# Performance work log

Hardware: AMD Instinct MI355X
Metric: run time of the kernel (lower is better)

## Reference

```python
import jax, jax.numpy as jnp
import numpy as np

D = 1024
H = 4
HD = D // H
B = 256
L = 64
DILATIONS = (1, 4, 8, 16)


def setup_inputs() -> dict:
    key = jax.random.key(0)
    ks = jax.random.split(key, 12)
    s = 1.0 / np.sqrt(D)
    return {
        "x": jax.random.normal(ks[0], (B, D), jnp.float32),
        "hist": jax.random.normal(ks[1], (L, B, D), jnp.float32),
        "Wq": jax.random.normal(ks[2], (D, D), jnp.float32) * s,
        "bq": jnp.zeros((D,), jnp.float32),
        "Wk": jax.random.normal(ks[3], (D, D), jnp.float32) * s,
        "bk": jnp.zeros((D,), jnp.float32),
        "Wv": jax.random.normal(ks[4], (D, D), jnp.float32) * s,
        "bv": jnp.zeros((D,), jnp.float32),
        "Wo": jax.random.normal(ks[5], (D, D), jnp.float32) * s,
        "bo": jnp.zeros((D,), jnp.float32),
        "dil_w": jnp.full((len(DILATIONS),), 1.0 / len(DILATIONS), jnp.float32),
        "gamma": jnp.ones((D,), jnp.float32),
        "beta": jnp.zeros((D,), jnp.float32),
    }


def reference(x, hist, Wq, bq, Wk, bk, Wv, bv, Wo, bo, dil_w, gamma, beta):
    scale = 1.0 / np.sqrt(HD)
    q = (x @ Wq + bq).reshape(B, H, HD)  # (B, H, HD)
    attended = []
    for d in DILATIONS:
        # history frames at stride d, concatenated along dim 0 (faithful to torch.cat)
        frames = hist[::d].reshape(-1, D)              # (T', D), T' = ceil(L/d)*B
        k = (frames @ Wk + bk).reshape(-1, H, HD)      # (T', H, HD)
        v = (frames @ Wv + bv).reshape(-1, H, HD)
        s = jnp.einsum('bhd,thd->bht', q, k) * scale   # (B, H, T')
        a = jax.nn.softmax(s, axis=-1)
        attended.append(jnp.einsum('bht,thd->bhd', a, v).reshape(B, D))
    w = jax.nn.softmax(dil_w, axis=0)
    combined = sum(w[i] * attended[i] for i in range(len(DILATIONS)))
    y = x + combined @ Wo + bo
    mu = jnp.mean(y, axis=-1, keepdims=True)
    var = jnp.var(y, axis=-1, keepdims=True)
    return (y - mu) / jnp.sqrt(var + 1e-5) * gamma + beta
```

## Files before the change

### kernel.cpp

```cpp
#include <hip/hip_runtime.h>


#define DD    1024
#define TALL  16384

typedef _Float16 half8  __attribute__((ext_vector_type(8)));
typedef _Float16 half4v __attribute__((ext_vector_type(4)));
typedef float    floatx4 __attribute__((ext_vector_type(4)));
typedef unsigned int u32;

static const size_t OFF_WOT  = 0;
static const size_t OFF_WV16 = 2097152;
static const size_t OFF_WK16 = 4194304;
static const size_t OFF_WQ16 = 6291456;
static const size_t OFF_XB   = 8388608;
static const size_t OFF_G    = 8912896;
static const size_t OFF_WVOT = 11010048;
static const size_t OFF_WQKT = 19398656;
static const size_t OFF_BVWO = 27787264;
static const size_t OFF_BQK  = 27791360;
static const size_t OFF_PHR  = 27807744;
static const size_t OFF_OPP  = 29904896;
static const size_t OFF_HB   = 38293504;
static const size_t OFF_HT   = 71848960;
static const size_t OFF_S    = 105403392;

__device__ __forceinline__ size_t chunk16_off(int g) {
  if (g < 4)  return (size_t)g * 2097152;
  if (g < 8)  return 19398656 + (size_t)(g - 4) * 2097152;
  if (g < 12) return 29904896 + (size_t)(g - 8) * 2097152;
  return 38293504 + (size_t)(g - 12) * 2097152;
}

__device__ __forceinline__ void gl_lds16(const void* g, void* l) {
  __builtin_amdgcn_global_load_lds((const __attribute__((address_space(1))) u32*)g,
                                   (__attribute__((address_space(3))) u32*)l, 16, 0, 0);
}

__global__ void prep_kernel(const float* __restrict__ Wo, const float* __restrict__ Wv,
                            const float* __restrict__ Wk, const float* __restrict__ Wq,
                            const float* __restrict__ x, const float* __restrict__ hist,
                            _Float16* __restrict__ WoT, _Float16* __restrict__ Wv16,
                            _Float16* __restrict__ Wk16, _Float16* __restrict__ Wq16,
                            _Float16* __restrict__ xb, _Float16* __restrict__ histb,
                            _Float16* __restrict__ histT) {
  int bid = blockIdx.x, tid = threadIdx.x;
  if (bid < 1024) {
    int k0 = (bid & 31) * 32, n0 = (bid >> 5) * 32;
    __shared__ float t32[32][33];
    int tx = tid & 31, ty = tid >> 5;
#pragma unroll
    for (int i = 0; i < 4; i++) {
      int r = ty + i * 8;
      t32[r][tx] = Wo[(size_t)(k0 + r) * DD + n0 + tx];
    }
    __syncthreads();
#pragma unroll
    for (int i = 0; i < 4; i++) {
      int r = ty + i * 8;
      WoT[(size_t)(n0 + r) * DD + k0 + tx] = (_Float16)t32[tx][r];
    }
  } else if (bid < 4352) {
    const float* src; _Float16* dst; size_t i;
    if (bid < 2048)      { src = Wv; dst = Wv16; i = (size_t)(bid - 1024) * 256 + tid; }
    else if (bid < 3072) { src = Wk; dst = Wk16; i = (size_t)(bid - 2048) * 256 + tid; }
    else if (bid < 4096) { src = Wq; dst = Wq16; i = (size_t)(bid - 3072) * 256 + tid; }
    else                 { src = x;  dst = xb;   i = (size_t)(bid - 4096) * 256 + tid; }
    float4 v = ((const float4*)src)[i];
    half4v h = {(_Float16)v.x, (_Float16)v.y, (_Float16)v.z, (_Float16)v.w};
    *(half4v*)(dst + 4 * i) = h;
  } else {
    int tb = bid - 4352;
    int t0 = (tb & 255) * 64, f0 = (tb >> 8) * 64;
    __shared__ _Float16 lt[64][72];
    int r = tid >> 2, c0 = (tid & 3) * 16;
    half8 s0, s1;
#pragma unroll
    for (int i = 0; i < 4; i++) {
      float4 v = *(const float4*)&hist[(size_t)(t0 + r) * 1024 + f0 + c0 + i * 4];
      half4v h = {(_Float16)v.x, (_Float16)v.y, (_Float16)v.z, (_Float16)v.w};
      *(half4v*)&lt[r][c0 + i * 4] = h;
      if (i < 2) { s0[i*4]=h[0]; s0[i*4+1]=h[1]; s0[i*4+2]=h[2]; s0[i*4+3]=h[3]; }
      else { s1[(i-2)*4]=h[0]; s1[(i-2)*4+1]=h[1]; s1[(i-2)*4+2]=h[2]; s1[(i-2)*4+3]=h[3]; }
    }
    *(half8*)&histb[(size_t)(t0 + r) * 1024 + f0 + c0] = s0;
    *(half8*)&histb[(size_t)(t0 + r) * 1024 + f0 + c0 + 8] = s1;
    __syncthreads();
    int fr = tid >> 2, tc0 = (tid & 3) * 16;
    half8 o0, o1;
#pragma unroll
    for (int j = 0; j < 8; j++) { o0[j] = lt[tc0 + j][fr]; o1[j] = lt[tc0 + 8 + j][fr]; }
    *(half8*)&histT[(size_t)(f0 + fr) * TALL + t0 + tc0] = o0;
    *(half8*)&histT[(size_t)(f0 + fr) * TALL + t0 + tc0 + 8] = o1;
  }
}

__device__ __forceinline__ void gemm_core(const _Float16* __restrict__ A, size_t lda,
                                          const _Float16* __restrict__ B, size_t ldb,
                                          int kIters, _Float16* As, _Float16* Bs,
                                          int tid, floatx4 acc[4][4]) {
  int lane = tid & 63, w = tid >> 6;
  int l15 = lane & 15, quad = lane >> 4;
  int wm = (w >> 1) * 64, wn = (w & 1) * 64;
  int swz = ((tid & 3) ^ ((tid >> 3) & 3)) * 8;
  int pch = (quad ^ ((l15 >> 1) & 3)) * 8;
  const char* gA0 = (const char*)(A + (size_t)(tid >> 2) * lda + swz);
  const char* gA1 = (const char*)(A + ((size_t)(tid >> 2) + 64) * lda + swz);
  const char* gB0 = (const char*)(B + (size_t)(tid >> 2) * ldb + swz);
  const char* gB1 = (const char*)(B + ((size_t)(tid >> 2) + 64) * ldb + swz);
  _Float16* lA = As + w * 512;
  _Float16* lB = Bs + w * 512;
#define GC_STAGE(buf, k)                                    \
  do {                                                      \
    size_t off_ = (size_t)(k) * 64;                         \
    gl_lds16(gA0 + off_, lA + (buf) * 4096);                \
    gl_lds16(gA1 + off_, lA + (buf) * 4096 + 2048);         \
    gl_lds16(gB0 + off_, lB + (buf) * 4096);                \
    gl_lds16(gB1 + off_, lB + (buf) * 4096 + 2048);         \
  } while (0)
#define GC_STEP(buf, k)                                                       \
  do {                                                                        \
    if ((k) + 1 < kIters) asm volatile("s_waitcnt vmcnt(4)" ::: "memory");    \
    else                  asm volatile("s_waitcnt vmcnt(0)" ::: "memory");    \
    asm volatile("s_barrier" ::: "memory");                                   \
    const _Float16* Ac_ = As + (buf) * 4096;                                  \
    const _Float16* Bc_ = Bs + (buf) * 4096;                                  \
    half8 a_[4];                                                              \
    _Pragma("unroll")                                                         \
    for (int mi = 0; mi < 4; mi++)                                            \
      a_[mi] = *(const half8*)&Ac_[(wm + mi * 16 + l15) * 32 + pch];          \
    _Pragma("unroll")                                                         \
    for (int ni = 0; ni < 4; ni++) {                                          \
      half8 b8_ = *(const half8*)&Bc_[(wn + ni * 16 + l15) * 32 + pch];       \
      _Pragma("unroll")                                                       \
      for (int mi = 0; mi < 4; mi++)                                          \
        acc[mi][ni] = __builtin_amdgcn_mfma_f32_16x16x32_f16(a_[mi], b8_,     \
                                                             acc[mi][ni], 0, 0, 0); \
    }                                                                         \
    asm volatile("s_waitcnt lgkmcnt(0)" ::: "memory");                        \
    asm volatile("s_barrier" ::: "memory");                                   \
    if ((k) + 2 < kIters) GC_STAGE(buf, (k) + 2);                             \
  } while (0)
  GC_STAGE(0, 0);
  GC_STAGE(1, 1);
  for (int kk = 0; kk < kIters; kk += 2) {
    GC_STEP(0, kk);
    GC_STEP(1, kk + 1);
  }
#undef GC_STEP
#undef GC_STAGE
}

__device__ __forceinline__ void gemm256_core(const _Float16* __restrict__ A, size_t lda,
                                             const _Float16* __restrict__ B, size_t ldb,
                                             int nT, _Float16* As, _Float16* Bs,
                                             int tid, floatx4 acc[8][4]) {
  int lane = tid & 63, w = tid >> 6;
  int l15 = lane & 15, quad = lane >> 4;
  int wr = w >> 2, wc = w & 3;
  int pch = (quad ^ ((l15 >> 1) & 3)) * 8;
  int srow = tid >> 2;
  int schunk = (tid & 3) ^ ((tid >> 3) & 3);
  const char* gA0 = (const char*)(A + (size_t)srow * lda + schunk * 8);
  const char* gA1 = (const char*)(A + (size_t)(srow + 128) * lda + schunk * 8);
  const char* gB0 = (const char*)(B + (size_t)srow * ldb + schunk * 8);
  const char* gB1 = (const char*)(B + (size_t)(srow + 128) * ldb + schunk * 8);
  _Float16* lA = As + w * 512;
  _Float16* lB = Bs + w * 512;
#define STA256(buf, t)                                        \
  do { size_t o_ = (size_t)(t) * 64;                          \
    gl_lds16(gA0 + o_, lA + (buf) * 8192);                    \
    gl_lds16(gA1 + o_, lA + (buf) * 8192 + 4096);             \
  } while (0)
#define STB256(buf, t)                                        \
  do { size_t o_ = (size_t)(t) * 64;                          \
    gl_lds16(gB0 + o_, lB + (buf) * 8192);                    \
    gl_lds16(gB1 + o_, lB + (buf) * 8192 + 4096);             \
  } while (0)
  STA256(0, 0); STB256(0, 0);
  if (nT > 1) { STA256(1, 1); STB256(1, 1); }
  if (nT > 2) { STA256(2, 2); STB256(2, 2); }
  for (int t = 0; t < nT; ++t) {
    int buf = t & 3;
    if (t + 2 < nT)      asm volatile("s_waitcnt vmcnt(8)" ::: "memory");
    else if (t + 1 < nT) asm volatile("s_waitcnt vmcnt(4)" ::: "memory");
    else                 asm volatile("s_waitcnt vmcnt(0)" ::: "memory");
    asm volatile("s_barrier" ::: "memory");
    const _Float16* Ac = As + buf * 8192;
    const _Float16* Bc = Bs + buf * 8192;
    half8 b8[4], a8[4];
#pragma unroll
    for (int ni = 0; ni < 4; ni++)
      b8[ni] = *(const half8*)&Bc[(wc * 64 + ni * 16 + l15) * 32 + pch];
#pragma unroll
    for (int mi = 0; mi < 4; mi++)
      a8[mi] = *(const half8*)&Ac[(wr * 128 + mi * 16 + l15) * 32 + pch];
    if (t + 3 < nT) STA256((t + 3) & 3, t + 3);
    asm volatile("s_barrier" ::: "memory");
    asm volatile("s_waitcnt lgkmcnt(0)" ::: "memory");
    __builtin_amdgcn_s_setprio(1);
#pragma unroll
    for (int mi = 0; mi < 4; mi++)
#pragma unroll
      for (int ni = 0; ni < 4; ni++)
        acc[mi][ni] = __builtin_amdgcn_mfma_f32_16x16x32_f16(a8[mi], b8[ni], acc[mi][ni], 0, 0, 0);
    __builtin_amdgcn_s_setprio(0);
    asm volatile("s_barrier" ::: "memory");
#pragma unroll
    for (int mi = 0; mi < 4; mi++)
      a8[mi] = *(const half8*)&Ac[(wr * 128 + 64 + mi * 16 + l15) * 32 + pch];
    if (t + 3 < nT) STB256((t + 3) & 3, t + 3);
    asm volatile("s_barrier" ::: "memory");
    asm volatile("s_waitcnt lgkmcnt(0)" ::: "memory");
    __builtin_amdgcn_s_setprio(1);
#pragma unroll
    for (int mi = 0; mi < 4; mi++)
#pragma unroll
      for (int ni = 0; ni < 4; ni++)
        acc[4 + mi][ni] = __builtin_amdgcn_mfma_f32_16x16x32_f16(a8[mi], b8[ni], acc[4 + mi][ni], 0, 0, 0);
    __builtin_amdgcn_s_setprio(0);
    asm volatile("s_barrier" ::: "memory");
  }
#undef STA256
#undef STB256
}

template <bool OUTF32>
__launch_bounds__(256, 3)
__global__ void gemm_f16_kernel(const _Float16* __restrict__ A, size_t lda, size_t aoffz,
                                const _Float16* __restrict__ B, size_t ldb, size_t boffz,
                                int kIters, const float* __restrict__ bias, size_t biasoffz,
                                float scale, void* __restrict__ C, size_t ldc, size_t coffz) {
  __shared__ __align__(16) _Float16 As[8192];
  __shared__ __align__(16) _Float16 Bs[8192];
  int tid = threadIdx.x;
  const _Float16* Ab = A + aoffz * blockIdx.z + (size_t)(blockIdx.y * 128) * lda;
  const _Float16* Bb = B + boffz * blockIdx.z + (size_t)(blockIdx.x * 128) * ldb;
  floatx4 acc[4][4];
  floatx4 zero = {0.f, 0.f, 0.f, 0.f};
#pragma unroll
  for (int a = 0; a < 4; a++)
#pragma unroll
    for (int b = 0; b < 4; b++) acc[a][b] = zero;
  gemm_core(Ab, lda, Bb, ldb, kIters, As, Bs, tid, acc);
  int lane = tid & 63, w = tid >> 6;
  int l15 = lane & 15, quad = lane >> 4;
  int wm = (w >> 1) * 64, wn = (w & 1) * 64;
#pragma unroll
  for (int mi = 0; mi < 4; mi++)
#pragma unroll
    for (int ni = 0; ni < 4; ni++) {
      int colg = blockIdx.x * 128 + wn + ni * 16 + l15;
      float bv = bias ? bias[biasoffz * blockIdx.z + colg] : 0.f;
#pragma unroll
      for (int r = 0; r < 4; r++) {
        int rowg = blockIdx.y * 128 + wm + mi * 16 + quad * 4 + r;
        float v = (acc[mi][ni][r] + bv) * scale;
        size_t idx = coffz * blockIdx.z + (size_t)rowg * ldc + colg;
        if (OUTF32) ((float*)C)[idx] = v;
        else ((_Float16*)C)[idx] = (_Float16)v;
      }
    }
}

__launch_bounds__(256, 3)
__global__ void wpack_kernel(const _Float16* __restrict__ WoT, const _Float16* __restrict__ Wv16,
                             const _Float16* __restrict__ Wk16, const _Float16* __restrict__ Wq16,
                             const float* __restrict__ bv, const float* __restrict__ bq,
                             _Float16* __restrict__ WVOT, _Float16* __restrict__ WQKT,
                             float* __restrict__ bvwo, float* __restrict__ bqk) {
  __shared__ __align__(16) _Float16 As[8192];
  __shared__ __align__(16) _Float16 Bs[8192];
  int bid = blockIdx.x, tid = threadIdx.x;
  if (bid < 512) {
    bool isQK = bid >= 256;
    int g = bid & 255;
    int x = g & 7, y = (g >> 3) & 7, z = g >> 6;
    const _Float16* A = isQK ? Wk16 : WoT;
    const _Float16* B = isQK ? Wq16 : Wv16;
    const _Float16* Ab = A + 256 * z + (size_t)(y * 128) * 1024;
    const _Float16* Bb = B + 256 * z + (size_t)(x * 128) * 1024;
    floatx4 acc[4][4];
    floatx4 zero = {0.f, 0.f, 0.f, 0.f};
#pragma unroll
    for (int a = 0; a < 4; a++)
#pragma unroll
      for (int b = 0; b < 4; b++) acc[a][b] = zero;
    gemm_core(Ab, 1024, Bb, 1024, 8, As, Bs, tid, acc);
    float scale = isQK ? 0.0625f : 1.0f;
    _Float16* C = isQK ? WQKT : WVOT;
    size_t ldc = isQK ? 1024 : 4096;
    size_t zoff = isQK ? (size_t)1048576 * z : (size_t)1024 * z;
    int lane = tid & 63, w = tid >> 6;
    int l15 = lane & 15, quad = lane >> 4;
    int wm = (w >> 1) * 64, wn = (w & 1) * 64;
#pragma unroll
    for (int mi = 0; mi < 4; mi++)
#pragma unroll
      for (int ni = 0; ni < 4; ni++) {
        int col = x * 128 + wn + ni * 16 + l15;
#pragma unroll
        for (int r = 0; r < 4; r++) {
          int row = y * 128 + wm + mi * 16 + quad * 4 + r;
          C[zoff + (size_t)row * ldc + col] = (_Float16)(acc[mi][ni][r] * scale);
        }
      }
  } else if (bid < 516) {
    int j = (bid - 512) * 256 + tid;
    const half8* row = (const half8*)(WoT + (size_t)j * 1024);
    float a = 0.f;
    for (int c = 0; c < 128; c++) {
      half8 w8 = row[c];
#pragma unroll
      for (int e = 0; e < 8; e++) a += bv[c * 8 + e] * (float)w8[e];
    }
    bvwo[j] = a;
  } else {
    int idx = (bid - 516) * 256 + tid;
    int h = idx >> 10, f = idx & 1023;
    const _Float16* row = Wk16 + (size_t)f * 1024 + h * 256;
    float a = 0.f;
    for (int n = 0; n < 256; n++) a += bq[h * 256 + n] * (float)row[n];
    bqk[idx] = a * 0.0625f;
  }
}

__launch_bounds__(512, 2)
__global__ void gemm256_s_kernel(const _Float16* __restrict__ G, const _Float16* __restrict__ histb,
                                 _Float16* __restrict__ S) {
  __shared__ __align__(16) _Float16 As[32768];
  __shared__ __align__(16) _Float16 Bs[32768];
  int bid = blockIdx.x, tid = threadIdx.x;
  int h = bid >> 6, nt = bid & 63;
  const _Float16* Ab = G + (size_t)h * 262144;
  const _Float16* Bb = histb + (size_t)(nt * 256) * 1024;
  floatx4 acc[8][4];
  floatx4 zero = {0.f, 0.f, 0.f, 0.f};
#pragma unroll
  for (int a = 0; a < 8; a++)
#pragma unroll
    for (int b = 0; b < 4; b++) acc[a][b] = zero;
  gemm256_core(Ab, 1024, Bb, 1024, 32, As, Bs, tid, acc);
  int lane = tid & 63, w = tid >> 6;
  int l15 = lane & 15, quad = lane >> 4;
  int wr = w >> 2, wc = w & 3;
#pragma unroll
  for (int mh = 0; mh < 2; mh++)
#pragma unroll
    for (int mi = 0; mi < 4; mi++)
#pragma unroll
      for (int ni = 0; ni < 4; ni++) {
        int col = nt * 256 + wc * 64 + ni * 16 + l15;
#pragma unroll
        for (int r = 0; r < 4; r++) {
          int row = wr * 128 + mh * 64 + mi * 16 + quad * 4 + r;
          S[(size_t)h * 4194304 + (size_t)row * TALL + col] = (_Float16)acc[mh * 4 + mi][ni][r];
        }
      }
}

__global__ void softmax_kernel(_Float16* __restrict__ S, const float* __restrict__ dil_w) {
  int r = blockIdx.x, tid = threadIdx.x;
  _Float16* row = S + (size_t)r * TALL;
  int lane = tid & 63;
  float ef[8][8];
  float es[8];
  __shared__ float Zf[64];
  __shared__ float Zd[4];
  __shared__ float cf[64];
#pragma unroll
  for (int i = 0; i < 8; i++) {
    half8 v = *(const half8*)&row[((size_t)i * 256 + tid) * 8];
    float s = 0.f;
#pragma unroll
    for (int j = 0; j < 8; j++) { float e = __expf((float)v[j]); ef[i][j] = e; s += e; }
#pragma unroll
    for (int off = 1; off <= 16; off <<= 1) s += __shfl_xor(s, off, 64);
    es[i] = s;
  }
  if ((lane & 31) == 0) {
    int half = tid >> 5;
#pragma unroll
    for (int i = 0; i < 8; i++) Zf[i * 8 + half] = es[i];
  }
  __syncthreads();
  if (tid < 4) {
    int step = 1 << (tid + (tid ? 1 : 0));
    float z = 0.f;
    for (int f = 0; f < 64; f += step) z += Zf[f];
    Zd[tid] = z;
  }
  __syncthreads();
  if (tid < 64) {
    float w0 = dil_w[0], w1 = dil_w[1], w2 = dil_w[2], w3 = dil_w[3];
    float wmx = fmaxf(fmaxf(w0, w1), fmaxf(w2, w3));
    float e0 = __expf(w0 - wmx), e1 = __expf(w1 - wmx), e2 = __expf(w2 - wmx), e3 = __expf(w3 - wmx);
    float wsum = e0 + e1 + e2 + e3;
    float c = (e0 / wsum) / Zd[0];
    if ((tid & 3) == 0) c += (e1 / wsum) / Zd[1];
    if ((tid & 7) == 0) c += (e2 / wsum) / Zd[2];
    if ((tid & 15) == 0) c += (e3 / wsum) / Zd[3];
    cf[tid] = c * 256.0f;
  }
  __syncthreads();
#pragma unroll
  for (int i = 0; i < 8; i++) {
    float c = cf[i * 8 + (tid >> 5)];
    half8 o;
#pragma unroll
    for (int j = 0; j < 8; j++) o[j] = (_Float16)(ef[i][j] * c);
    *(half8*)&row[((size_t)i * 256 + tid) * 8] = o;
  }
}

__launch_bounds__(512, 2)
__global__ void gemm256_ph_kernel(const _Float16* __restrict__ P, const _Float16* __restrict__ histT,
                                  char* __restrict__ ws) {
  __shared__ __align__(16) _Float16 As[32768];
  __shared__ __align__(16) _Float16 Bs[32768];
  int bid = blockIdx.x, tid = threadIdx.x;
  int xcd = bid & 7, slot = bid >> 3;
  int g = xcd + 8 * (slot >> 4);
  int member = slot & 15;
  int h = member >> 2, nt = member & 3;
  const _Float16* Ab = P + (size_t)h * 4194304 + (size_t)g * 1024;
  const _Float16* Bb = histT + (size_t)(nt * 256) * TALL + (size_t)g * 1024;
  floatx4 acc[8][4];
  floatx4 zero = {0.f, 0.f, 0.f, 0.f};
#pragma unroll
  for (int a = 0; a < 8; a++)
#pragma unroll
    for (int b = 0; b < 4; b++) acc[a][b] = zero;
  gemm256_core(Ab, TALL, Bb, TALL, 32, As, Bs, tid, acc);
  _Float16* chunk = (_Float16*)(ws + chunk16_off(g));
  int lane = tid & 63, w = tid >> 6;
  int l15 = lane & 15, quad = lane >> 4;
  int wr = w >> 2, wc = w & 3;
#pragma unroll
  for (int mh = 0; mh < 2; mh++)
#pragma unroll
    for (int mi = 0; mi < 4; mi++)
#pragma unroll
      for (int ni = 0; ni < 4; ni++) {
        int col = h * 1024 + nt * 256 + wc * 64 + ni * 16 + l15;
#pragma unroll
        for (int r = 0; r < 4; r++) {
          int row = wr * 128 + mh * 64 + mi * 16 + quad * 4 + r;
          chunk[(size_t)row * 4096 + col] = (_Float16)acc[mh * 4 + mi][ni][r];
        }
      }
}

__global__ void reduce_ph_kernel(const char* __restrict__ ws, _Float16* __restrict__ PHred) {
  size_t e8 = ((size_t)blockIdx.x * 256 + threadIdx.x) * 8;
  float s[8] = {0.f, 0.f, 0.f, 0.f, 0.f, 0.f, 0.f, 0.f};
#pragma unroll
  for (int g = 0; g < 16; g++) {
    const _Float16* p = (const _Float16*)(ws + chunk16_off(g));
    half8 v = *(const half8*)&p[e8];
#pragma unroll
    for (int j = 0; j < 8; j++) s[j] += (float)v[j];
  }
  half8 o;
#pragma unroll
  for (int j = 0; j < 8; j++) o[j] = (_Float16)s[j];
  *(half8*)&PHred[e8] = o;
}

__global__ void ln_kernel(const float* __restrict__ x, const float* __restrict__ part2,
                          const float* __restrict__ bo, const float* __restrict__ bvwo,
                          const float* __restrict__ gamma, const float* __restrict__ beta,
                          float* __restrict__ out) {
  int b = blockIdx.x, t = threadIdx.x;
  __shared__ float red[8];
  float y[4];
  float sum = 0.f, sq = 0.f;
#pragma unroll
  for (int i = 0; i < 4; i++) {
    int j = t + i * 256;
    float v = x[(size_t)b * 1024 + j] + bo[j] + bvwo[j];
#pragma unroll
    for (int z = 0; z < 8; z++) v += part2[(size_t)z * 262144 + (size_t)b * 1024 + j];
    y[i] = v;
    sum += v;
    sq += v * v;
  }
#pragma unroll
  for (int off = 1; off < 64; off <<= 1) {
    sum += __shfl_xor(sum, off, 64);
    sq += __shfl_xor(sq, off, 64);
  }
  int w = t >> 6, lane = t & 63;
  if (lane == 0) { red[w] = sum; red[4 + w] = sq; }
  __syncthreads();
  sum = red[0] + red[1] + red[2] + red[3];
  sq = red[4] + red[5] + red[6] + red[7];
  float mu = sum * (1.f / 1024.f);
  float var = sq * (1.f / 1024.f) - mu * mu;
  float inv = rsqrtf(var + 1e-5f);
#pragma unroll
  for (int i = 0; i < 4; i++) {
    int j = t + i * 256;
    out[(size_t)b * 1024 + j] = (y[i] - mu) * inv * gamma[j] + beta[j];
  }
}

extern "C" void kernel_launch(void* const* d_in, const int* in_sizes, int n_in,
                              void* d_out, int out_size, void* d_ws, size_t ws_size,
                              hipStream_t stream) {
  const float* x     = (const float*)d_in[0];
  const float* hist  = (const float*)d_in[1];
  const float* Wq    = (const float*)d_in[2];
  const float* bq    = (const float*)d_in[3];
  const float* Wk    = (const float*)d_in[4];
  const float* Wv    = (const float*)d_in[6];
  const float* bv    = (const float*)d_in[7];
  const float* Wo    = (const float*)d_in[8];
  const float* bo    = (const float*)d_in[9];
  const float* dil_w = (const float*)d_in[10];
  const float* gamma = (const float*)d_in[11];
  const float* beta  = (const float*)d_in[12];
  char* ws = (char*)d_ws;

  _Float16* WoT   = (_Float16*)(ws + OFF_WOT);
  _Float16* Wv16  = (_Float16*)(ws + OFF_WV16);
  _Float16* Wk16  = (_Float16*)(ws + OFF_WK16);
  _Float16* Wq16  = (_Float16*)(ws + OFF_WQ16);
  _Float16* xb    = (_Float16*)(ws + OFF_XB);
  _Float16* G     = (_Float16*)(ws + OFF_G);
  _Float16* WVOT  = (_Float16*)(ws + OFF_WVOT);
  _Float16* WQKT  = (_Float16*)(ws + OFF_WQKT);
  float* bvwo     = (float*)(ws + OFF_BVWO);
  float* bqk      = (float*)(ws + OFF_BQK);
  _Float16* PHred = (_Float16*)(ws + OFF_PHR);
  float* oppart   = (float*)(ws + OFF_OPP);
  _Float16* histb = (_Float16*)(ws + OFF_HB);
  _Float16* histT = (_Float16*)(ws + OFF_HT);
  _Float16* Sb    = (_Float16*)(ws + OFF_S);

  prep_kernel<<<dim3(8448), 256, 0, stream>>>(Wo, Wv, Wk, Wq, x, hist,
                                              WoT, Wv16, Wk16, Wq16, xb, histb, histT);
  wpack_kernel<<<dim3(532), 256, 0, stream>>>(WoT, Wv16, Wk16, Wq16, bv, bq,
                                              WVOT, WQKT, bvwo, bqk);
  gemm_f16_kernel<false><<<dim3(8, 2, 4), 256, 0, stream>>>(
      xb, 1024, 0, WQKT, 1024, 1048576, 32, bqk, 1024, 1.0f, (void*)G, 1024, 262144);
  gemm256_s_kernel<<<dim3(256), 512, 0, stream>>>(G, histb, Sb);
  softmax_kernel<<<dim3(1024), 256, 0, stream>>>(Sb, dil_w);
  gemm256_ph_kernel<<<dim3(256), 512, 0, stream>>>(Sb, histT, ws);
  reduce_ph_kernel<<<dim3(512), 256, 0, stream>>>(ws, PHred);
  gemm_f16_kernel<true><<<dim3(8, 2, 8), 256, 0, stream>>>(
      PHred, 4096, 512, WVOT, 4096, 512, 16, nullptr, 0, 1.0f / 256.0f,
      (void*)oppart, 1024, 262144);
  ln_kernel<<<dim3(256), 256, 0, stream>>>(x, oppart, bo, bvwo, gamma, beta, (float*)d_out);
}
```

Before: 322.8 us.

## Fuse exp into score GEMM epilogue and scale probabilities inside PH GEMM

After: 323.4 us. Within noise of the previous version (+0.2%).

```diff
diff --git a/kernel.cpp b/kernel.cpp
--- a/kernel.cpp
+++ b/kernel.cpp
@@ -327,9 +327,10 @@
 
 __launch_bounds__(512, 2)
 __global__ void gemm256_s_kernel(const _Float16* __restrict__ G, const _Float16* __restrict__ histb,
-                                 _Float16* __restrict__ S) {
-  __shared__ __align__(16) _Float16 As[32768];
-  __shared__ __align__(16) _Float16 Bs[32768];
+                                 _Float16* __restrict__ Eout, float* __restrict__ zframe) {
+  __shared__ __align__(16) _Float16 SM[65536];
+  _Float16* As = SM;
+  _Float16* Bs = SM + 32768;
   int bid = blockIdx.x, tid = threadIdx.x;
   int h = bid >> 6, nt = bid & 63;
   const _Float16* Ab = G + (size_t)h * 262144;
@@ -344,111 +345,187 @@
   int lane = tid & 63, w = tid >> 6;
   int l15 = lane & 15, quad = lane >> 4;
   int wr = w >> 2, wc = w & 3;
+  __syncthreads();
 #pragma unroll
   for (int mh = 0; mh < 2; mh++)
 #pragma unroll
     for (int mi = 0; mi < 4; mi++)
 #pragma unroll
       for (int ni = 0; ni < 4; ni++) {
-        int col = nt * 256 + wc * 64 + ni * 16 + l15;
+        int col = wc * 64 + ni * 16 + l15;
 #pragma unroll
         for (int r = 0; r < 4; r++) {
           int row = wr * 128 + mh * 64 + mi * 16 + quad * 4 + r;
-          S[(size_t)h * 4194304 + (size_t)row * TALL + col] = (_Float16)acc[mh * 4 + mi][ni][r];
+          SM[row * 256 + col] = (_Float16)__expf(acc[mh * 4 + mi][ni][r]);
         }
       }
-}
-
-__global__ void softmax_kernel(_Float16* __restrict__ S, const float* __restrict__ dil_w) {
-  int r = blockIdx.x, tid = threadIdx.x;
-  _Float16* row = S + (size_t)r * TALL;
-  int lane = tid & 63;
-  float ef[8][8];
-  float es[8];
-  __shared__ float Zf[64];
-  __shared__ float Zd[4];
-  __shared__ float cf[64];
-#pragma unroll
-  for (int i = 0; i < 8; i++) {
-    half8 v = *(const half8*)&row[((size_t)i * 256 + tid) * 8];
+  __syncthreads();
+  int c32 = lane & 31, hs = lane >> 5;
+#pragma unroll
+  for (int it = 0; it < 16; it++) {
+    int row = w * 32 + it * 2 + hs;
+    half8 v = *(const half8*)&SM[row * 256 + c32 * 8];
     float s = 0.f;
 #pragma unroll
-    for (int j = 0; j < 8; j++) { float e = __expf((float)v[j]); ef[i][j] = e; s += e; }
+    for (int j = 0; j < 8; j++) s += (float)v[j];
 #pragma unroll
     for (int off = 1; off <= 16; off <<= 1) s += __shfl_xor(s, off, 64);
-    es[i] = s;
-  }
-  if ((lane & 31) == 0) {
-    int half = tid >> 5;
-#pragma unroll
-    for (int i = 0; i < 8; i++) Zf[i * 8 + half] = es[i];
-  }
-  __syncthreads();
-  if (tid < 4) {
-    int step = 1 << (tid + (tid ? 1 : 0));
-    float z = 0.f;
-    for (int f = 0; f < 64; f += step) z += Zf[f];
-    Zd[tid] = z;
-  }
-  __syncthreads();
-  if (tid < 64) {
-    float w0 = dil_w[0], w1 = dil_w[1], w2 = dil_w[2], w3 = dil_w[3];
-    float wmx = fmaxf(fmaxf(w0, w1), fmaxf(w2, w3));
-    float e0 = __expf(w0 - wmx), e1 = __expf(w1 - wmx), e2 = __expf(w2 - wmx), e3 = __expf(w3 - wmx);
-    float wsum = e0 + e1 + e2 + e3;
-    float c = (e0 / wsum) / Zd[0];
-    if ((tid & 3) == 0) c += (e1 / wsum) / Zd[1];
-    if ((tid & 7) == 0) c += (e2 / wsum) / Zd[2];
-    if ((tid & 15) == 0) c += (e3 / wsum) / Zd[3];
-    cf[tid] = c * 256.0f;
-  }
-  __syncthreads();
-#pragma unroll
-  for (int i = 0; i < 8; i++) {
-    float c = cf[i * 8 + (tid >> 5)];
-    half8 o;
-#pragma unroll
-    for (int j = 0; j < 8; j++) o[j] = (_Float16)(ef[i][j] * c);
-    *(half8*)&row[((size_t)i * 256 + tid) * 8] = o;
+    *(half8*)&Eout[(size_t)h * 4194304 + (size_t)row * TALL + nt * 256 + c32 * 8] = v;
+    if (c32 == 0) zframe[(size_t)(h * 256 + row) * 64 + nt] = s;
+  }
+}
+
+__global__ void csoftmax_kernel(const float* __restrict__ zframe, const float* __restrict__ dil_w,
+                                float* __restrict__ ctab) {
+  int row = blockIdx.x * 256 + threadIdx.x;
+  const float* z = zframe + (size_t)row * 64;
+  float z1 = 0.f, z4 = 0.f, z8 = 0.f, z16 = 0.f;
+#pragma unroll
+  for (int f = 0; f < 64; f++) {
+    float v = z[f];
+    z1 += v;
+    if (!(f & 3))  z4 += v;
+    if (!(f & 7))  z8 += v;
+    if (!(f & 15)) z16 += v;
+  }
+  float w0 = dil_w[0], w1 = dil_w[1], w2 = dil_w[2], w3 = dil_w[3];
+  float wmx = fmaxf(fmaxf(w0, w1), fmaxf(w2, w3));
+  float e0 = __expf(w0 - wmx), e1 = __expf(w1 - wmx), e2 = __expf(w2 - wmx), e3 = __expf(w3 - wmx);
+  float wsum = e0 + e1 + e2 + e3;
+  float b0 = (e0 / wsum) / z1 * 256.0f;
+  float b1 = (e1 / wsum) / z4 * 256.0f;
+  float b2 = (e2 / wsum) / z8 * 256.0f;
+  float b3 = (e3 / wsum) / z16 * 256.0f;
+  float* c = ctab + (size_t)row * 64;
+#pragma unroll
+  for (int f = 0; f < 64; f++) {
+    float cv = b0;
+    if (!(f & 3))  cv += b1;
+    if (!(f & 7))  cv += b2;
+    if (!(f & 15)) cv += b3;
+    c[f] = cv;
   }
 }
 
 __launch_bounds__(512, 2)
-__global__ void gemm256_ph_kernel(const _Float16* __restrict__ P, const _Float16* __restrict__ histT,
-                                  char* __restrict__ ws) {
-  __shared__ __align__(16) _Float16 As[32768];
-  __shared__ __align__(16) _Float16 Bs[32768];
+__global__ void gemm256_ph_kernel(const _Float16* __restrict__ E, const _Float16* __restrict__ histT,
+                                  const float* __restrict__ ctab, char* __restrict__ ws) {
+  __shared__ __align__(16) _Float16 SM[65536];
+  _Float16* As = SM;
+  _Float16* Bs = SM + 16384;
   int bid = blockIdx.x, tid = threadIdx.x;
   int xcd = bid & 7, slot = bid >> 3;
   int g = xcd + 8 * (slot >> 4);
   int member = slot & 15;
   int h = member >> 2, nt = member & 3;
-  const _Float16* Ab = P + (size_t)h * 4194304 + (size_t)g * 1024;
-  const _Float16* Bb = histT + (size_t)(nt * 256) * TALL + (size_t)g * 1024;
-  floatx4 acc[8][4];
-  floatx4 zero = {0.f, 0.f, 0.f, 0.f};
-#pragma unroll
-  for (int a = 0; a < 8; a++)
-#pragma unroll
-    for (int b = 0; b < 4; b++) acc[a][b] = zero;
-  gemm256_core(Ab, TALL, Bb, TALL, 32, As, Bs, tid, acc);
-  _Float16* chunk = (_Float16*)(ws + chunk16_off(g));
   int lane = tid & 63, w = tid >> 6;
   int l15 = lane & 15, quad = lane >> 4;
   int wr = w >> 2, wc = w & 3;
+  int pch = (quad ^ ((l15 >> 1) & 3)) * 8;
+  int srow = tid >> 2;
+  int schunk = (tid & 3) ^ ((tid >> 3) & 3);
+  const _Float16* gA = E + (size_t)h * 4194304 + (size_t)g * 1024 + (size_t)srow * TALL + schunk * 8;
+  const _Float16* gB = histT + (size_t)(nt * 256) * TALL + (size_t)g * 1024 + (size_t)srow * TALL + schunk * 8;
+  const float* cr0 = ctab + (size_t)(h * 256 + srow) * 64 + g * 4;
+  const float* cr1 = cr0 + (size_t)128 * 64;
+  _Float16* lA = As + w * 512 + lane * 8;
+  _Float16* lB = Bs + w * 512 + lane * 8;
+  floatx4 acc[8][4];
+  floatx4 zero = {0.f, 0.f, 0.f, 0.f};
+#pragma unroll
+  for (int a = 0; a < 8; a++)
+#pragma unroll
+    for (int b = 0; b < 4; b++) acc[a][b] = zero;
+  half8 xa0, xa1, xb0, xb1; float xc0, xc1;
+  half8 ya0, ya1, yb0, yb1; float yc0, yc1;
+#define PH_LOAD(P, t)                                                         \
+  do { size_t o_ = (size_t)(t) * 32;                                          \
+    P##a0 = *(const half8*)(gA + o_);                                         \
+    P##a1 = *(const half8*)(gA + o_ + (size_t)128 * TALL);                    \
+    P##b0 = *(const half8*)(gB + o_);                                         \
+    P##b1 = *(const half8*)(gB + o_ + (size_t)128 * TALL);                    \
+    P##c0 = cr0[(t) >> 3]; P##c1 = cr1[(t) >> 3];                             \
+  } while (0)
+#define PH_COMPUTE(b)                                                         \
+  do {                                                                        \
+    const _Float16* Ac_ = As + (b) * 8192;                                    \
+    const _Float16* Bc_ = Bs + (b) * 8192;                                    \
+    half8 bb_[4], aa_[4];                                                     \
+    _Pragma("unroll")                                                         \
+    for (int ni = 0; ni < 4; ni++)                                            \
+      bb_[ni] = *(const half8*)&Bc_[(wc * 64 + ni * 16 + l15) * 32 + pch];    \
+    _Pragma("unroll")                                                         \
+    for (int mi = 0; mi < 4; mi++)                                            \
+      aa_[mi] = *(const half8*)&Ac_[(wr * 128 + mi * 16 + l15) * 32 + pch];   \
+    __builtin_amdgcn_s_setprio(1);                                            \
+    _Pragma("unroll")                                                         \
+    for (int mi = 0; mi < 4; mi++) {                                          \
+      _Pragma("unroll")                                                       \
+      for (int ni = 0; ni < 4; ni++)                                          \
+        acc[mi][ni] = __builtin_amdgcn_mfma_f32_16x16x32_f16(aa_[mi], bb_[ni], acc[mi][ni], 0, 0, 0); \
+    }                                                                         \
+    __builtin_amdgcn_s_setprio(0);                                            \
+    _Pragma("unroll")                                                         \
+    for (int mi = 0; mi < 4; mi++)                                            \
+      aa_[mi] = *(const half8*)&Ac_[(wr * 128 + 64 + mi * 16 + l15) * 32 + pch]; \
+    __builtin_amdgcn_s_setprio(1);                                            \
+    _Pragma("unroll")                                                         \
+    for (int mi = 0; mi < 4; mi++) {                                          \
+      _Pragma("unroll")                                                       \
+      for (int ni = 0; ni < 4; ni++)                                          \
+        acc[4 + mi][ni] = __builtin_amdgcn_mfma_f32_16x16x32_f16(aa_[mi], bb_[ni], acc[4 + mi][ni], 0, 0, 0); \
+    }                                                                         \
+    __builtin_amdgcn_s_setprio(0);                                            \
+  } while (0)
+#define PH_STEP(P, N, t, b)                                                   \
+  do {                                                                        \
+    if ((t) + 1 < 32) PH_LOAD(N, (t) + 1);                                    \
+    _Float16 ch0_ = (_Float16)P##c0, ch1_ = (_Float16)P##c1;                  \
+    half8 w0_, w1_;                                                           \
+    _Pragma("unroll")                                                         \
+    for (int j = 0; j < 8; j++) { w0_[j] = P##a0[j] * ch0_; w1_[j] = P##a1[j] * ch1_; } \
+    *(half8*)(lA + (b) * 8192) = w0_;                                         \
+    *(half8*)(lA + (b) * 8192 + 4096) = w1_;                                  \
+    *(half8*)(lB + (b) * 8192) = P##b0;                                       \
+    *(half8*)(lB + (b) * 8192 + 4096) = P##b1;                                \
+    asm volatile("s_waitcnt lgkmcnt(0)" ::: "memory");                        \
+    asm volatile("s_barrier" ::: "memory");                                   \
+    PH_COMPUTE(b);                                                            \
+    asm volatile("s_waitcnt lgkmcnt(0)" ::: "memory");                        \
+    asm volatile("s_barrier" ::: "memory");                                   \
+  } while (0)
+  PH_LOAD(x, 0);
+  for (int t = 0; t < 32; t += 2) {
+    PH_STEP(x, y, t, 0);
+    PH_STEP(y, x, t + 1, 1);
+  }
+#undef PH_STEP
+#undef PH_COMPUTE
+#undef PH_LOAD
+  __syncthreads();
 #pragma unroll
   for (int mh = 0; mh < 2; mh++)
 #pragma unroll
     for (int mi = 0; mi < 4; mi++)
 #pragma unroll
       for (int ni = 0; ni < 4; ni++) {
-        int col = h * 1024 + nt * 256 + wc * 64 + ni * 16 + l15;
+        int col = wc * 64 + ni * 16 + l15;
 #pragma unroll
         for (int r = 0; r < 4; r++) {
           int row = wr * 128 + mh * 64 + mi * 16 + quad * 4 + r;
-          chunk[(size_t)row * 4096 + col] = (_Float16)acc[mh * 4 + mi][ni][r];
+          SM[row * 256 + col] = (_Float16)acc[mh * 4 + mi][ni][r];
         }
       }
+  __syncthreads();
+  _Float16* chunk = (_Float16*)(ws + chunk16_off(g));
+  int c32 = lane & 31, hs = lane >> 5;
+  int colbase = h * 1024 + nt * 256;
+#pragma unroll
+  for (int it = 0; it < 16; it++) {
+    int row = w * 32 + it * 2 + hs;
+    half8 v = *(const half8*)&SM[row * 256 + c32 * 8];
+    *(half8*)&chunk[(size_t)row * 4096 + colbase + c32 * 8] = v;
+  }
 }
 
 __global__ void reduce_ph_kernel(const char* __restrict__ ws, _Float16* __restrict__ PHred) {
@@ -536,7 +613,9 @@
   float* oppart   = (float*)(ws + OFF_OPP);
   _Float16* histb = (_Float16*)(ws + OFF_HB);
   _Float16* histT = (_Float16*)(ws + OFF_HT);
-  _Float16* Sb    = (_Float16*)(ws + OFF_S);
+  _Float16* Eb    = (_Float16*)(ws + OFF_S);
+  float* zframe   = (float*)(ws + OFF_WQKT);
+  float* ctab     = (float*)(ws + OFF_G);
 
   prep_kernel<<<dim3(8448), 256, 0, stream>>>(Wo, Wv, Wk, Wq, x, hist,
                                               WoT, Wv16, Wk16, Wq16, xb, histb, histT);
@@ -544,9 +623,9 @@
                                               WVOT, WQKT, bvwo, bqk);
   gemm_f16_kernel<false><<<dim3(8, 2, 4), 256, 0, stream>>>(
       xb, 1024, 0, WQKT, 1024, 1048576, 32, bqk, 1024, 1.0f, (void*)G, 1024, 262144);
-  gemm256_s_kernel<<<dim3(256), 512, 0, stream>>>(G, histb, Sb);
-  softmax_kernel<<<dim3(1024), 256, 0, stream>>>(Sb, dil_w);
-  gemm256_ph_kernel<<<dim3(256), 512, 0, stream>>>(Sb, histT, ws);
+  gemm256_s_kernel<<<dim3(256), 512, 0, stream>>>(G, histb, Eb, zframe);
+  csoftmax_kernel<<<dim3(4), 256, 0, stream>>>(zframe, dil_w, ctab);
+  gemm256_ph_kernel<<<dim3(256), 512, 0, stream>>>(Eb, histT, ctab, ws);
   reduce_ph_kernel<<<dim3(512), 256, 0, stream>>>(ws, PHred);
   gemm_f16_kernel<true><<<dim3(8, 2, 8), 256, 0, stream>>>(
       PHred, 4096, 512, WVOT, 4096, 512, 16, nullptr, 0, 1.0f / 256.0f,
```
